# Optimization experiments

Measured on AMD Instinct MI355X. Metric: run time of the kernel, lower is better.

Reference implementation:

```python
import jax, jax.numpy as jnp
import numpy as np

B, T, U, V = 8, 128, 64, 512
BLANK = 0
NEG_INF = -1e30  # finite 'log zero' to keep gradients NaN-free


def setup_inputs() -> dict:
    key = jax.random.key(0)
    k1, k2, k3, k4, k5 = jax.random.split(key, 5)
    emissions = jax.random.normal(k1, (B, T, V), dtype=jnp.float32)
    predictions = jax.random.normal(k2, (B, U, V), dtype=jnp.float32)
    labels = jax.random.randint(k3, (B, U - 1), 1, V, dtype=jnp.int32)
    # max(input_lengths) must equal T; max(label_lengths) must equal U-1
    input_lengths = jax.random.randint(k4, (B,), T // 2, T + 1, dtype=jnp.int32).at[0].set(T)
    label_lengths = jax.random.randint(k5, (B,), (U - 1) // 2, U, dtype=jnp.int32).at[0].set(U - 1)
    return {
        "emissions": emissions,
        "predictions": predictions,
        "labels": labels,
        "input_lengths": input_lengths,
        "label_lengths": label_lengths,
    }


def _rnnt_costs(emissions, predictions, labels, input_lengths, label_lengths, blank=BLANK):
    b, t_len, v = emissions.shape
    u_len = predictions.shape[1]
    # joint lattice log-probs: log_softmax over vocab of additive joint
    log_probs = jax.nn.log_softmax(
        emissions[:, :, None, :] + predictions[:, None, :, :], axis=-1
    )  # (B, T, U, V)
    blank_lp = log_probs[..., blank]  # (B, T, U)
    lbl = jnp.broadcast_to(labels[:, None, :, None], (b, t_len, u_len - 1, 1))
    label_lp = jnp.take_along_axis(log_probs[:, :, : u_len - 1, :], lbl, axis=3)[..., 0]  # (B,T,U-1)

    def step(a_top, xs):
        # a_top[b,u] = alpha[t-1,u] + blank_lp[t-1,u]  (entry-from-above scores)
        blank_t, label_t = xs  # (B,U), (B,U-1)
        # c[u] = sum_{k<u} label_lp[t,k]  -> alpha[t,u] = c[u] + LSE_{u'<=u}(a_top[u'] - c[u'])
        c = jnp.concatenate(
            [jnp.zeros((b, 1), a_top.dtype), jnp.cumsum(label_t, axis=1)], axis=1
        )  # (B, U)
        alpha_t = c + jax.lax.cumlogsumexp(a_top - c, axis=1)
        a_next = alpha_t + blank_t  # alpha[t,u] + blank_lp[t,u]
        return a_next, a_next

    a0 = jnp.full((b, u_len), NEG_INF, dtype=emissions.dtype).at[:, 0].set(0.0)
    xs = (jnp.moveaxis(blank_lp, 1, 0), jnp.moveaxis(label_lp, 1, 0))
    _, scores = jax.lax.scan(step, a0, xs)  # (T, B, U): alpha[t,u]+blank_lp[t,u]
    scores = jnp.moveaxis(scores, 1, 0)  # (B, T, U)
    bidx = jnp.arange(b)
    # cost_b = -(alpha[T_b-1, U_b] + blank_lp[T_b-1, U_b])
    costs = -scores[bidx, input_lengths - 1, label_lengths]
    return costs


def reference(emissions, predictions, labels, input_lengths, label_lengths):
    return _rnnt_costs(emissions, predictions, labels, input_lengths, label_lengths)
```

## Files before the change

kernel.cpp:

```cpp
#include <hip/hip_runtime.h>

#define B 8
#define T 128
#define U 64
#define V 512
#define ROWS (T + 2)
#define LN2 0.6931471805599453f

template<int CTRL, int ROWM>
__device__ __forceinline__ float dpp_movf(float x, int old_bits) {
    int r = __builtin_amdgcn_update_dpp(old_bits, __builtin_bit_cast(int, x),
                                        CTRL, ROWM, 0xF, false);
    return __builtin_bit_cast(float, r);
}
__device__ __forceinline__ float wave_sum63(float x) {
    x += dpp_movf<0x111, 0xF>(x, 0);
    x += dpp_movf<0x112, 0xF>(x, 0);
    x += dpp_movf<0x114, 0xF>(x, 0);
    x += dpp_movf<0x118, 0xF>(x, 0);
    x += dpp_movf<0x142, 0xA>(x, 0);
    x += dpp_movf<0x143, 0xC>(x, 0);
    return x;
}
__device__ __forceinline__ float wave_max63(float x) {
    const int NI = (int)0xff800000u;
    x = fmaxf(x, dpp_movf<0x111, 0xF>(x, NI));
    x = fmaxf(x, dpp_movf<0x112, 0xF>(x, NI));
    x = fmaxf(x, dpp_movf<0x114, 0xF>(x, NI));
    x = fmaxf(x, dpp_movf<0x118, 0xF>(x, NI));
    x = fmaxf(x, dpp_movf<0x142, 0xA>(x, NI));
    x = fmaxf(x, dpp_movf<0x143, 0xC>(x, NI));
    return x;
}
__device__ __forceinline__ float rdlane(float x, int lane) {
    return __builtin_bit_cast(float,
        __builtin_amdgcn_readlane(__builtin_bit_cast(int, x), lane));
}
__device__ __forceinline__ float dpp_shr1(float x) {
    int r = __builtin_amdgcn_update_dpp(0, __builtin_bit_cast(int, x),
                                        0x138, 0xF, 0xF, false);
    return __builtin_bit_cast(float, r);
}

__global__ __launch_bounds__(256) void lp_kernel(
    const float* __restrict__ em, const float* __restrict__ pr,
    const int* __restrict__ labels,
    float* __restrict__ blankP, float* __restrict__ labelP)
{
    __shared__ float Pexp[32][V];

    const int bid  = blockIdx.x;
    const int ug   = bid & 1;
    const int tg   = (bid >> 1) & 15;
    const int b    = bid >> 5;
    const int lane = threadIdx.x & 63;
    const int wave = threadIdx.x >> 6;

    #pragma unroll 2
    for (int r = 0; r < 8; ++r) {
        const int ul = wave * 8 + r;
        const int gu = ug * 32 + ul;
        const float* prow = pr + ((size_t)b * U + gu) * V;
        const float4 xa = ((const float4*)prow)[lane];
        const float4 xb = ((const float4*)prow)[64 + lane];
        float m = fmaxf(fmaxf(fmaxf(xa.x, xa.y), fmaxf(xa.z, xa.w)),
                        fmaxf(fmaxf(xb.x, xb.y), fmaxf(xb.z, xb.w)));
        const float mp = rdlane(wave_max63(m), 63);
        float4 oa, ob;
        oa.x = __expf(xa.x - mp); oa.y = __expf(xa.y - mp);
        oa.z = __expf(xa.z - mp); oa.w = __expf(xa.w - mp);
        ob.x = __expf(xb.x - mp); ob.y = __expf(xb.y - mp);
        ob.z = __expf(xb.z - mp); ob.w = __expf(xb.w - mp);
        ((float4*)&Pexp[ul][0])[lane]      = oa;
        ((float4*)&Pexp[ul][0])[64 + lane] = ob;
    }
    __syncthreads();

    const int t0 = tg * 8 + wave * 2;
    const int t1 = t0 + 1;
    const float* er0 = em + ((size_t)b * T + t0) * V;
    const float* er1 = em + ((size_t)b * T + t1) * V;
    const float4 ea0 = ((const float4*)er0)[lane];
    const float4 eb0 = ((const float4*)er0)[64 + lane];
    const float4 ea1 = ((const float4*)er1)[lane];
    const float4 eb1 = ((const float4*)er1)[64 + lane];
    float m0 = fmaxf(fmaxf(fmaxf(ea0.x, ea0.y), fmaxf(ea0.z, ea0.w)),
                     fmaxf(fmaxf(eb0.x, eb0.y), fmaxf(eb0.z, eb0.w)));
    float m1 = fmaxf(fmaxf(fmaxf(ea1.x, ea1.y), fmaxf(ea1.z, ea1.w)),
                     fmaxf(fmaxf(eb1.x, eb1.y), fmaxf(eb1.z, eb1.w)));
    const float me0 = rdlane(wave_max63(m0), 63);
    const float me1 = rdlane(wave_max63(m1), 63);
    float E0[8], E1[8];
    E0[0] = __expf(ea0.x - me0); E0[1] = __expf(ea0.y - me0);
    E0[2] = __expf(ea0.z - me0); E0[3] = __expf(ea0.w - me0);
    E0[4] = __expf(eb0.x - me0); E0[5] = __expf(eb0.y - me0);
    E0[6] = __expf(eb0.z - me0); E0[7] = __expf(eb0.w - me0);
    E1[0] = __expf(ea1.x - me1); E1[1] = __expf(ea1.y - me1);
    E1[2] = __expf(ea1.z - me1); E1[3] = __expf(ea1.w - me1);
    E1[4] = __expf(eb1.x - me1); E1[5] = __expf(eb1.y - me1);
    E1[6] = __expf(eb1.z - me1); E1[7] = __expf(eb1.w - me1);

    float S0 = 1.0f, S1 = 1.0f;
    #pragma unroll 2
    for (int ul = 0; ul < 32; ++ul) {
        const float4 pa = ((const float4*)&Pexp[ul][0])[lane];
        const float4 pb = ((const float4*)&Pexp[ul][0])[64 + lane];
        float p0 = E0[0] * pa.x;
        p0 = fmaf(E0[1], pa.y, p0); p0 = fmaf(E0[2], pa.z, p0);
        p0 = fmaf(E0[3], pa.w, p0); p0 = fmaf(E0[4], pb.x, p0);
        p0 = fmaf(E0[5], pb.y, p0); p0 = fmaf(E0[6], pb.z, p0);
        p0 = fmaf(E0[7], pb.w, p0);
        float p1 = E1[0] * pa.x;
        p1 = fmaf(E1[1], pa.y, p1); p1 = fmaf(E1[2], pa.z, p1);
        p1 = fmaf(E1[3], pa.w, p1); p1 = fmaf(E1[4], pb.x, p1);
        p1 = fmaf(E1[5], pb.y, p1); p1 = fmaf(E1[6], pb.z, p1);
        p1 = fmaf(E1[7], pb.w, p1);
        const float s0 = rdlane(wave_sum63(p0), 63);
        const float s1 = rdlane(wave_sum63(p1), 63);
        if (lane == ul) { S0 = s0; S1 = s1; }
    }

    if (lane < 32) {
        const int gu = ug * 32 + lane;
        const float Ppb = Pexp[lane][0];
        const float r0 = 1.0f / S0, r1 = 1.0f / S1;
        const float ebl0 = __expf(er0[0] - me0);
        const float ebl1 = __expf(er1[0] - me1);
        const size_t o0 = ((size_t)b * T + t0) * U + gu;
        const size_t o1 = o0 + U;
        blankP[o0] = ebl0 * Ppb * r0;
        blankP[o1] = ebl1 * Ppb * r1;
        if (gu < U - 1) {
            const int lb = labels[b * (U - 1) + gu];
            const float Ppl = Pexp[lane][lb];
            labelP[o0] = __expf(er0[lb] - me0) * Ppl * r0;
            labelP[o1] = __expf(er1[lb] - me1) * Ppl * r1;
        }
    }
}

__global__ __launch_bounds__(256) void alpha_kernel(
    const float* __restrict__ blankP, const float* __restrict__ labelP,
    const int* __restrict__ in_len, const int* __restrict__ lab_len,
    float* __restrict__ out)
{
    __shared__ float2 QI[ROWS * U];

    const int b   = blockIdx.x;
    const int tid = threadIdx.x;

    const float* gb = blankP + (size_t)b * T * U;
    const float* gl = labelP + (size_t)b * T * U;
    for (int i = tid; i < ROWS * U; i += 256) {
        const int r = i >> 6, u = i & 63;
        const float x = (r >= 1 && r <= T) ? gb[(r - 1) * U + u] : 0.0f;
        const float y = (r <= T - 1 && u >= 1) ? gl[r * U + u - 1] : 0.0f;
        QI[i] = make_float2(x, y);
    }
    __syncthreads();
    if (tid >= 64) return;

    const int u  = tid;
    const int Tb = in_len[b];
    const int Ub = lab_len[b];
    const int dmax = (Tb - 1) + Ub;

    auto qidx = [&](int d) {
        int r = d - u;
        r = min(max(r, 0), T + 1);
        return r * U + u;
    };

    float A = (u == 0) ? 1.0f : 0.0f;
    int   off = 0;
    float aCap = 1.0f;
    int   offCap = 0;
    float sPend = 1.0f;
    int   ePend = 0;

    float2 c8[8], n8[8];
    #pragma unroll
    for (int j = 0; j < 8; ++j) c8[j] = QI[qidx(1 + j)];

    for (int d0 = 1; d0 <= 185; d0 += 8) {
        #pragma unroll
        for (int j = 0; j < 8; ++j) {
            n8[j] = QI[qidx(d0 + 8 + j)];
            A = fmaf(A, c8[j].x, dpp_shr1(A) * c8[j].y);
            if ((j & 3) == 3) {
                A *= sPend;
                off += ePend;
                const float mx = rdlane(wave_max63(A), 63);
                int e = ((__builtin_bit_cast(int, mx) >> 23) & 255) - 127;
                e = max(e, -96);
                sPend = __builtin_bit_cast(float, (157 - e) << 23);
                ePend = e - 30;
            }
            const bool cap = (d0 + j == dmax);
            aCap   = cap ? A   : aCap;
            offCap = cap ? off : offCap;
        }
        #pragma unroll
        for (int j = 0; j < 8; ++j) c8[j] = n8[j];
    }

    if (u == Ub) {
        const float bprob = QI[Tb * U + u].x;
        out[b] = -(__log2f(aCap) + (float)offCap + __log2f(bprob)) * LN2;
    }
}

extern "C" void kernel_launch(void* const* d_in, const int* in_sizes, int n_in,
                              void* d_out, int out_size, void* d_ws, size_t ws_size,
                              hipStream_t stream) {
    const float* em      = (const float*)d_in[0];
    const float* pr      = (const float*)d_in[1];
    const int*   labels  = (const int*)d_in[2];
    const int*   in_len  = (const int*)d_in[3];
    const int*   lab_len = (const int*)d_in[4];
    float* out = (float*)d_out;

    float* blankP = (float*)d_ws;
    float* labelP = blankP + (size_t)B * T * U;

    lp_kernel<<<B * T / 4, 256, 0, stream>>>(em, pr, labels, blankP, labelP);
    alpha_kernel<<<B, 256, 0, stream>>>(blankP, labelP, in_len, lab_len, out);
}
```

Before: 31.84 us.

## Fuse lattice probability and alpha recursion into one MFMA-based kernel per batch

Merges the two kernels into a single kernel with one block per batch element. The softmax normaliser sum over vocab, exp(em) dotted with exp(pr), is computed with bf16 MFMA using a hi/lo split (three products) to approximate fp32 precision. The probabilities go straight into shared memory for the alpha recursion instead of through a global workspace. This removes a launch and the global round trip, but uses only 8 blocks, so the matmul phase runs on very few CUs. It also drops max-subtraction in the exps, which risks overflow for large inputs.

```diff
diff --git a/kernel.cpp b/kernel.cpp
--- a/kernel.cpp
+++ b/kernel.cpp
@@ -5,22 +5,17 @@
 #define U 64
 #define V 512
 #define ROWS (T + 2)
+#define PADK 520
 #define LN2 0.6931471805599453f
+
+typedef __attribute__((ext_vector_type(8))) short bf8v;
+typedef __attribute__((ext_vector_type(4))) float f4v;
 
 template<int CTRL, int ROWM>
 __device__ __forceinline__ float dpp_movf(float x, int old_bits) {
     int r = __builtin_amdgcn_update_dpp(old_bits, __builtin_bit_cast(int, x),
                                         CTRL, ROWM, 0xF, false);
     return __builtin_bit_cast(float, r);
-}
-__device__ __forceinline__ float wave_sum63(float x) {
-    x += dpp_movf<0x111, 0xF>(x, 0);
-    x += dpp_movf<0x112, 0xF>(x, 0);
-    x += dpp_movf<0x114, 0xF>(x, 0);
-    x += dpp_movf<0x118, 0xF>(x, 0);
-    x += dpp_movf<0x142, 0xA>(x, 0);
-    x += dpp_movf<0x143, 0xC>(x, 0);
-    return x;
 }
 __device__ __forceinline__ float wave_max63(float x) {
     const int NI = (int)0xff800000u;
@@ -42,120 +37,122 @@
     return __builtin_bit_cast(float, r);
 }
 
-__global__ __launch_bounds__(256) void lp_kernel(
+__device__ __forceinline__ short f2bf(float x) {
+    unsigned b = __builtin_bit_cast(unsigned, x);
+    unsigned r = (b + 0x7FFFu + ((b >> 16) & 1u)) >> 16;
+    return (short)r;
+}
+__device__ __forceinline__ float bf2f(short h) {
+    return __builtin_bit_cast(float, ((unsigned)(unsigned short)h) << 16);
+}
+
+__global__ __launch_bounds__(256) void fused_kernel(
     const float* __restrict__ em, const float* __restrict__ pr,
     const int* __restrict__ labels,
-    float* __restrict__ blankP, float* __restrict__ labelP)
-{
-    __shared__ float Pexp[32][V];
-
-    const int bid  = blockIdx.x;
-    const int ug   = bid & 1;
-    const int tg   = (bid >> 1) & 15;
-    const int b    = bid >> 5;
-    const int lane = threadIdx.x & 63;
-    const int wave = threadIdx.x >> 6;
-
-    #pragma unroll 2
-    for (int r = 0; r < 8; ++r) {
-        const int ul = wave * 8 + r;
-        const int gu = ug * 32 + ul;
-        const float* prow = pr + ((size_t)b * U + gu) * V;
-        const float4 xa = ((const float4*)prow)[lane];
-        const float4 xb = ((const float4*)prow)[64 + lane];
-        float m = fmaxf(fmaxf(fmaxf(xa.x, xa.y), fmaxf(xa.z, xa.w)),
-                        fmaxf(fmaxf(xb.x, xb.y), fmaxf(xb.z, xb.w)));
-        const float mp = rdlane(wave_max63(m), 63);
-        float4 oa, ob;
-        oa.x = __expf(xa.x - mp); oa.y = __expf(xa.y - mp);
-        oa.z = __expf(xa.z - mp); oa.w = __expf(xa.w - mp);
-        ob.x = __expf(xb.x - mp); ob.y = __expf(xb.y - mp);
-        ob.z = __expf(xb.z - mp); ob.w = __expf(xb.w - mp);
-        ((float4*)&Pexp[ul][0])[lane]      = oa;
-        ((float4*)&Pexp[ul][0])[64 + lane] = ob;
-    }
-    __syncthreads();
-
-    const int t0 = tg * 8 + wave * 2;
-    const int t1 = t0 + 1;
-    const float* er0 = em + ((size_t)b * T + t0) * V;
-    const float* er1 = em + ((size_t)b * T + t1) * V;
-    const float4 ea0 = ((const float4*)er0)[lane];
-    const float4 eb0 = ((const float4*)er0)[64 + lane];
-    const float4 ea1 = ((const float4*)er1)[lane];
-    const float4 eb1 = ((const float4*)er1)[64 + lane];
-    float m0 = fmaxf(fmaxf(fmaxf(ea0.x, ea0.y), fmaxf(ea0.z, ea0.w)),
-                     fmaxf(fmaxf(eb0.x, eb0.y), fmaxf(eb0.z, eb0.w)));
-    float m1 = fmaxf(fmaxf(fmaxf(ea1.x, ea1.y), fmaxf(ea1.z, ea1.w)),
-                     fmaxf(fmaxf(eb1.x, eb1.y), fmaxf(eb1.z, eb1.w)));
-    const float me0 = rdlane(wave_max63(m0), 63);
-    const float me1 = rdlane(wave_max63(m1), 63);
-    float E0[8], E1[8];
-    E0[0] = __expf(ea0.x - me0); E0[1] = __expf(ea0.y - me0);
-    E0[2] = __expf(ea0.z - me0); E0[3] = __expf(ea0.w - me0);
-    E0[4] = __expf(eb0.x - me0); E0[5] = __expf(eb0.y - me0);
-    E0[6] = __expf(eb0.z - me0); E0[7] = __expf(eb0.w - me0);
-    E1[0] = __expf(ea1.x - me1); E1[1] = __expf(ea1.y - me1);
-    E1[2] = __expf(ea1.z - me1); E1[3] = __expf(ea1.w - me1);
-    E1[4] = __expf(eb1.x - me1); E1[5] = __expf(eb1.y - me1);
-    E1[6] = __expf(eb1.z - me1); E1[7] = __expf(eb1.w - me1);
-
-    float S0 = 1.0f, S1 = 1.0f;
-    #pragma unroll 2
-    for (int ul = 0; ul < 32; ++ul) {
-        const float4 pa = ((const float4*)&Pexp[ul][0])[lane];
-        const float4 pb = ((const float4*)&Pexp[ul][0])[64 + lane];
-        float p0 = E0[0] * pa.x;
-        p0 = fmaf(E0[1], pa.y, p0); p0 = fmaf(E0[2], pa.z, p0);
-        p0 = fmaf(E0[3], pa.w, p0); p0 = fmaf(E0[4], pb.x, p0);
-        p0 = fmaf(E0[5], pb.y, p0); p0 = fmaf(E0[6], pb.z, p0);
-        p0 = fmaf(E0[7], pb.w, p0);
-        float p1 = E1[0] * pa.x;
-        p1 = fmaf(E1[1], pa.y, p1); p1 = fmaf(E1[2], pa.z, p1);
-        p1 = fmaf(E1[3], pa.w, p1); p1 = fmaf(E1[4], pb.x, p1);
-        p1 = fmaf(E1[5], pb.y, p1); p1 = fmaf(E1[6], pb.z, p1);
-        p1 = fmaf(E1[7], pb.w, p1);
-        const float s0 = rdlane(wave_sum63(p0), 63);
-        const float s1 = rdlane(wave_sum63(p1), 63);
-        if (lane == ul) { S0 = s0; S1 = s1; }
-    }
-
-    if (lane < 32) {
-        const int gu = ug * 32 + lane;
-        const float Ppb = Pexp[lane][0];
-        const float r0 = 1.0f / S0, r1 = 1.0f / S1;
-        const float ebl0 = __expf(er0[0] - me0);
-        const float ebl1 = __expf(er1[0] - me1);
-        const size_t o0 = ((size_t)b * T + t0) * U + gu;
-        const size_t o1 = o0 + U;
-        blankP[o0] = ebl0 * Ppb * r0;
-        blankP[o1] = ebl1 * Ppb * r1;
-        if (gu < U - 1) {
-            const int lb = labels[b * (U - 1) + gu];
-            const float Ppl = Pexp[lane][lb];
-            labelP[o0] = __expf(er0[lb] - me0) * Ppl * r0;
-            labelP[o1] = __expf(er1[lb] - me1) * Ppl * r1;
-        }
-    }
-}
-
-__global__ __launch_bounds__(256) void alpha_kernel(
-    const float* __restrict__ blankP, const float* __restrict__ labelP,
     const int* __restrict__ in_len, const int* __restrict__ lab_len,
     float* __restrict__ out)
 {
-    __shared__ float2 QI[ROWS * U];
-
-    const int b   = blockIdx.x;
-    const int tid = threadIdx.x;
-
-    const float* gb = blankP + (size_t)b * T * U;
-    const float* gl = labelP + (size_t)b * T * U;
-    for (int i = tid; i < ROWS * U; i += 256) {
-        const int r = i >> 6, u = i & 63;
-        const float x = (r >= 1 && r <= T) ? gb[(r - 1) * U + u] : 0.0f;
-        const float y = (r <= T - 1 && u >= 1) ? gl[r * U + u - 1] : 0.0f;
-        QI[i] = make_float2(x, y);
+    __shared__ __align__(16) char smemRaw[2 * 64 * PADK * 2];
+    __shared__ float Pp0s[U], Ppls[U], Ee0s[T];
+    __shared__ int   lbls[U];
+
+    short*  Ph = (short*)smemRaw;
+    short*  Pl = Ph + 64 * PADK;
+    float2* QI = (float2*)smemRaw;
+
+    const int b    = blockIdx.x;
+    const int tid  = threadIdx.x;
+    const int lane = tid & 63;
+    const int w    = tid >> 6;
+
+    if (tid < T)     Ee0s[tid] = __expf(em[((size_t)b * T + tid) * V]);
+    if (tid < U)     Pp0s[tid] = __expf(pr[((size_t)b * U + tid) * V]);
+    if (tid < U - 1) {
+        const int lb = labels[b * (U - 1) + tid];
+        lbls[tid] = lb;
+        Ppls[tid] = __expf(pr[((size_t)b * U + tid) * V + lb]);
+    }
+
+    for (int idx = tid; idx < 64 * 64; idx += 256) {
+        const int u = idx >> 6, c = idx & 63;
+        const float* prow = pr + ((size_t)b * U + u) * V + c * 8;
+        const float4 f0 = ((const float4*)prow)[0];
+        const float4 f1 = ((const float4*)prow)[1];
+        const float e[8] = {f0.x, f0.y, f0.z, f0.w, f1.x, f1.y, f1.z, f1.w};
+        bf8v hi, lo;
+        #pragma unroll
+        for (int j = 0; j < 8; ++j) {
+            const float x = __expf(e[j]);
+            const short h = f2bf(x);
+            hi[j] = h;
+            lo[j] = f2bf(x - bf2f(h));
+        }
+        ((bf8v*)Ph)[u * (PADK / 8) + c] = hi;
+        ((bf8v*)Pl)[u * (PADK / 8) + c] = lo;
+    }
+    __syncthreads();
+
+    f4v acc[2][4];
+    #pragma unroll
+    for (int i = 0; i < 2; ++i)
+        #pragma unroll
+        for (int n = 0; n < 4; ++n) acc[i][n] = (f4v){0.f, 0.f, 0.f, 0.f};
+
+    const int arow = lane & 15;
+    const int kb   = (lane >> 4) * 8;
+
+    #pragma unroll
+    for (int mtl = 0; mtl < 2; ++mtl) {
+        const int t = (w * 2 + mtl) * 16 + arow;
+        const float* erow = em + ((size_t)b * T + t) * V;
+        #pragma unroll 2
+        for (int ks = 0; ks < 16; ++ks) {
+            const int k0 = ks * 32 + kb;
+            const float4 f0 = ((const float4*)(erow + k0))[0];
+            const float4 f1 = ((const float4*)(erow + k0))[1];
+            const float e[8] = {f0.x, f0.y, f0.z, f0.w, f1.x, f1.y, f1.z, f1.w};
+            bf8v ah, al;
+            #pragma unroll
+            for (int j = 0; j < 8; ++j) {
+                const float x = __expf(e[j]);
+                const short h = f2bf(x);
+                ah[j] = h;
+                al[j] = f2bf(x - bf2f(h));
+            }
+            #pragma unroll
+            for (int nt = 0; nt < 4; ++nt) {
+                const int bu = nt * 16 + arow;
+                const bf8v bh = ((const bf8v*)Ph)[bu * (PADK / 8) + k0 / 8];
+                const bf8v bl = ((const bf8v*)Pl)[bu * (PADK / 8) + k0 / 8];
+                acc[mtl][nt] = __builtin_amdgcn_mfma_f32_16x16x32_bf16(ah, bh, acc[mtl][nt], 0, 0, 0);
+                acc[mtl][nt] = __builtin_amdgcn_mfma_f32_16x16x32_bf16(ah, bl, acc[mtl][nt], 0, 0, 0);
+                acc[mtl][nt] = __builtin_amdgcn_mfma_f32_16x16x32_bf16(al, bh, acc[mtl][nt], 0, 0, 0);
+            }
+        }
+    }
+    __syncthreads();
+
+    for (int i = tid; i < ROWS * U; i += 256) QI[i] = make_float2(0.f, 0.f);
+    __syncthreads();
+
+    const int ccol  = lane & 15;
+    const int crow0 = (lane >> 4) * 4;
+    #pragma unroll
+    for (int mtl = 0; mtl < 2; ++mtl) {
+        #pragma unroll
+        for (int nt = 0; nt < 4; ++nt) {
+            const int u = nt * 16 + ccol;
+            #pragma unroll
+            for (int r = 0; r < 4; ++r) {
+                const int t = (w * 2 + mtl) * 16 + crow0 + r;
+                const float inv = 1.0f / acc[mtl][nt][r];
+                QI[(t + 1) * U + u].x = Ee0s[t] * Pp0s[u] * inv;
+                if (u < U - 1) {
+                    const float eel = __expf(em[((size_t)b * T + t) * V + lbls[u]]);
+                    QI[t * U + (u + 1)].y = eel * Ppls[u] * inv;
+                }
+            }
+        }
     }
     __syncthreads();
     if (tid >= 64) return;
@@ -220,9 +217,5 @@
     const int*   lab_len = (const int*)d_in[4];
     float* out = (float*)d_out;
 
-    float* blankP = (float*)d_ws;
-    float* labelP = blankP + (size_t)B * T * U;
-
-    lp_kernel<<<B * T / 4, 256, 0, stream>>>(em, pr, labels, blankP, labelP);
-    alpha_kernel<<<B, 256, 0, stream>>>(blankP, labelP, in_len, lab_len, out);
-}
+    fused_kernel<<<B, 256, 0, stream>>>(em, pr, labels, in_len, lab_len, out);
+}
```

Measured after the change: 33.86 us. 6.3% more time.
